# Kernel tuning notes

Hardware: AMD Instinct MI355X
Metric: run time of the kernel (lower is better)

The kernel has to match this reference:

```python
import jax, jax.numpy as jnp
import numpy as np

B, S, DIM, FF = 64, 577, 768, 3072
BLK = 8          # block_shape = (8, 8)
DENSITY = 0.1    # fraction of 8x8 blocks that are nonzero


def _expand_block_mask(m):
    # m: [out//BLK, in//BLK] bool -> [out, in] float mask
    return jnp.repeat(jnp.repeat(m, BLK, axis=0), BLK, axis=1)


def setup_inputs() -> dict:
    key = jax.random.key(0)
    ks = jax.random.split(key, 7)
    x = jax.random.normal(ks[0], (B, S, DIM), dtype=jnp.float32)
    # nn.Linear-style init scale
    W1 = jax.random.normal(ks[1], (FF, DIM), dtype=jnp.float32) / np.sqrt(DIM).astype(np.float32)
    b1 = jax.random.normal(ks[2], (FF,), dtype=jnp.float32) * 0.02
    W2 = jax.random.normal(ks[3], (DIM, FF), dtype=jnp.float32) / np.sqrt(FF).astype(np.float32)
    b2 = jax.random.normal(ks[4], (DIM,), dtype=jnp.float32) * 0.02
    mask1 = jax.random.uniform(ks[5], (FF // BLK, DIM // BLK)) < DENSITY
    mask2 = jax.random.uniform(ks[6], (DIM // BLK, FF // BLK)) < DENSITY
    return {"x": x, "W1": W1, "b1": b1, "W2": W2, "b2": b2,
            "mask1": mask1, "mask2": mask2}


def reference(x, W1, b1, W2, b2, mask1, mask2):
    # fc1: block-sparse linear  y = x @ (W1 * M1)^T + b1
    Wm1 = W1 * _expand_block_mask(mask1).astype(W1.dtype)  # [FF, DIM]
    h = jnp.einsum('bsd,fd->bsf', x, Wm1) + b1             # [B, S, FF]
    h = jax.nn.gelu(h, approximate=False)                  # F.gelu default (exact)
    # fc2: block-sparse linear
    Wm2 = W2 * _expand_block_mask(mask2).astype(W2.dtype)  # [DIM, FF]
    return jnp.einsum('bsf,df->bsd', h, Wm2) + b2          # [B, S, DIM]
```

## Files before the change

### kernel.cpp

```cpp
#include <hip/hip_runtime.h>
#include <hip/hip_bf16.h>


typedef __attribute__((ext_vector_type(8))) short short8;
typedef __attribute__((ext_vector_type(4))) float f32x4;
typedef unsigned long long u64;
typedef unsigned short ushort_t;

#define DIM 768
#define FF 3072
#define NF16 192
#define ND16 48
#define NDB 96
#define NFB 384
#define MR 32
#define NT 1024
#define XP 776
#define HP 1544
#define XSEC (16 * XP)
#define HSEC (16 * HP)

#define S1CAP (NF16 * 96 + 32)
#define S2CAP (ND16 * 2 * 192 + 32)
#define W1S_TOT (S1CAP * 128)
#define W2S_TOT (S2CAP * 128)

#define MFMA __builtin_amdgcn_mfma_f32_16x16x32_bf16

__device__ __forceinline__ float gelu_fast(float v) {
    float t2 = v * fmaf(v * v, -0.10295667f, -2.30235629f);
    return v / (1.0f + exp2f(t2));
}
__device__ __forceinline__ ushort_t f2bs(float f) {
    union { __hip_bfloat16 h; ushort_t u; } cv;
    cv.h = __float2bfloat16(f);
    return cv.u;
}

__global__ __launch_bounds__(64)
void prep_count(const int* __restrict__ mask1, const int* __restrict__ mask2,
                int* __restrict__ off1, int* __restrict__ off2)
{
    const int l = threadIdx.x;
    const int g = blockIdx.x;
    if (g < NF16) {
        const int* r0 = mask1 + (2 * g) * NDB;
        const int* r1 = r0 + NDB;
        bool ua = (r0[l] | r1[l]) != 0;
        u64 ba = __ballot(ua);
        bool ub = (l < 32) && ((r0[64 + l] | r1[64 + l]) != 0);
        u64 bb = __ballot(ub);
        if (l == 0) {
            int cnt = __popcll(ba) + __popcll(bb);
            off1[g + 1] = (cnt + 15) & ~15;
        }
    } else {
        const int G = g - NF16;
        const int* r0 = mask2 + (2 * G) * NFB;
        const int* r1 = r0 + NFB;
        int c0 = 0, c1 = 0;
        #pragma unroll
        for (int p = 0; p < 6; ++p) {
            u64 b = __ballot((r0[p * 64 + l] | r1[p * 64 + l]) != 0);
            if (p < 3) c0 += __popcll(b); else c1 += __popcll(b);
        }
        if (l == 0) {
            off2[0 * ND16 + G + 1] = (c0 + 15) & ~15;
            off2[1 * ND16 + G + 1] = (c1 + 15) & ~15;
        }
    }
}

__global__ __launch_bounds__(64)
void prep_scan(int* __restrict__ off1, int* __restrict__ off2,
               ushort_t* __restrict__ idx1s, ushort_t* __restrict__ idx2s)
{
    if (threadIdx.x == 0) {
        off1[0] = 0;
        for (int i = 0; i < NF16; ++i) off1[i + 1] += off1[i];
        int e = off1[NF16];
        for (int i = 0; i < 32; ++i) idx1s[e + i] = 0;
    } else if (threadIdx.x == 1) {
        off2[0] = 0;
        for (int i = 0; i < 2 * ND16; ++i) off2[i + 1] += off2[i];
        int e = off2[2 * ND16];
        for (int i = 0; i < 32; ++i) idx2s[e + i] = 0;
    }
}

__global__ __launch_bounds__(256)
void prep_gather(const float* __restrict__ W1, const float* __restrict__ W2,
                 const int* __restrict__ mask1, const int* __restrict__ mask2,
                 const int* __restrict__ off1, const int* __restrict__ off2,
                 __hip_bfloat16* __restrict__ w1s, __hip_bfloat16* __restrict__ w2s,
                 ushort_t* __restrict__ idx1s, ushort_t* __restrict__ idx2s)
{
    __shared__ ushort_t sidx[192];
    __shared__ int sc[1];
    const int tid = threadIdx.x;
    const int l = tid & 63;
    const int g = blockIdx.x;

    if (g < NF16) {
        const int F = g;
        const int* r0 = mask1 + (2 * F) * NDB;
        const int* r1 = r0 + NDB;
        if (tid < 64) {
            bool ua = (r0[l] | r1[l]) != 0;
            u64 ba = __ballot(ua);
            bool ub = (l < 32) && ((r0[64 + l] | r1[64 + l]) != 0);
            u64 bb = __ballot(ub);
            int ca = __popcll(ba);
            if (ua) sidx[__popcll(ba & ((1ull << l) - 1ull))] = (ushort_t)l;
            if (ub) sidx[ca + __popcll(bb & ((1ull << l) - 1ull))] = (ushort_t)(64 + l);
            int cnt = ca + __popcll(bb);
            if (l == 0) {
                sc[0] = cnt;
                int cntp = (cnt + 15) & ~15;
                for (int i = cnt; i < cntp && i < 192; ++i) sidx[i] = 0;
            }
        }
        __syncthreads();
        const int cnt = sc[0];
        const int base = off1[F];
        const int cntp = off1[F + 1] - base;
        if (tid < cntp) idx1s[base + tid] = sidx[tid];
        for (int e = tid; e < cntp * 128; e += 256) {
            int slot = e >> 7, r = (e >> 3) & 15, j = e & 7;
            int db = sidx[slot];
            float w = 0.f;
            if (slot < cnt && mask1[(2 * F + (r >> 3)) * NDB + db])
                w = W1[(long)(F * 16 + r) * DIM + db * 8 + j];
            w1s[(long)base * 128 + e] = __float2bfloat16(w);
        }
    } else {
        const int gi = g - NF16;
        const int c = gi / ND16;
        const int G = gi % ND16;
        const int* r0 = mask2 + (2 * G) * NFB;
        const int* r1 = r0 + NFB;
        if (tid < 64) {
            u64 b[3]; int pc[3];
            #pragma unroll
            for (int p = 0; p < 3; ++p) {
                int fb = c * 192 + p * 64 + l;
                b[p] = __ballot((r0[fb] | r1[fb]) != 0);
                pc[p] = __popcll(b[p]);
            }
            int basea = 0;
            #pragma unroll
            for (int p = 0; p < 3; ++p) {
                if ((b[p] >> l) & 1ull)
                    sidx[basea + __popcll(b[p] & ((1ull << l) - 1ull))] = (ushort_t)(p * 64 + l);
                basea += pc[p];
            }
            if (l == 0) {
                int cnt = basea;
                sc[0] = cnt;
                int cntp = (cnt + 15) & ~15;
                for (int i = cnt; i < cntp && i < 192; ++i) sidx[i] = 0;
            }
        }
        __syncthreads();
        const int cnt = sc[0];
        const int base = off2[c * ND16 + G];
        const int cntp = off2[c * ND16 + G + 1] - base;
        if (tid < cntp) idx2s[base + tid] = sidx[tid];
        for (int e = tid; e < cntp * 128; e += 256) {
            int slot = e >> 7, r = (e >> 3) & 15, j = e & 7;
            int lfb = sidx[slot];
            int fb = c * 192 + lfb;
            float w = 0.f;
            if (slot < cnt && mask2[(2 * G + (r >> 3)) * NFB + fb])
                w = W2[(long)(G * 16 + r) * FF + fb * 8 + j];
            w2s[(long)base * 128 + e] = __float2bfloat16(w);
        }
    }
}

#define PREF(BUF, IP, WP, ARR, ROWOFF, SECOFF)                          \
    {                                                                   \
        uint4 q = *(const uint4*)(IP);                                  \
        unsigned dd0 = (lg & 2) ? q.y : q.x;                            \
        unsigned dd1 = (lg & 2) ? q.w : q.z;                            \
        int mo0 = (int)((dd0 >> shsel) & 0xffffu) * 8;                  \
        int mo1 = (int)((dd1 >> shsel) & 0xffffu) * 8;                  \
        BUF##a0 = *(const short8*)&ARR[ROWOFF + mo0];                   \
        BUF##a1 = *(const short8*)&ARR[ROWOFF + SECOFF + mo0];          \
        BUF##a2 = *(const short8*)&ARR[ROWOFF + mo1];                   \
        BUF##a3 = *(const short8*)&ARR[ROWOFF + SECOFF + mo1];          \
        BUF##w0 = *(const short8*)(WP);                                 \
        BUF##w1 = *(const short8*)(WP + 512);                           \
    }

#define PAIRSTEP(IP, WP, ARR, ROWOFF, SECOFF)                           \
    {                                                                   \
        short8 t0 = Aa0, t1 = Aa1, t2 = Aa2, t3 = Aa3, u0 = Aw0, u1 = Aw1; \
        PREF(A, IP, WP, ARR, ROWOFF, SECOFF)                            \
        ca = MFMA(t0, u0, ca, 0, 0, 0); cc = MFMA(t1, u0, cc, 0, 0, 0); \
        cb = MFMA(t2, u1, cb, 0, 0, 0); cd = MFMA(t3, u1, cd, 0, 0, 0); \
    }                                                                   \
    {                                                                   \
        short8 t0 = Ba0, t1 = Ba1, t2 = Ba2, t3 = Ba3, u0 = Bw0, u1 = Bw1; \
        PREF(B, (IP + 8), (WP + 1024), ARR, ROWOFF, SECOFF)             \
        ca = MFMA(t0, u0, ca, 0, 0, 0); cc = MFMA(t1, u0, cc, 0, 0, 0); \
        cb = MFMA(t2, u1, cb, 0, 0, 0); cd = MFMA(t3, u1, cd, 0, 0, 0); \
    }                                                                   \
    IP += 16; WP += 2048; s += 16;

__global__ __launch_bounds__(NT, 4)
void bsffn_main(const float* __restrict__ x,
                const float* __restrict__ pb1, const float* __restrict__ pb2,
                const ushort_t* __restrict__ w1s, const ushort_t* __restrict__ w2s,
                const ushort_t* __restrict__ idx1s, const ushort_t* __restrict__ idx2s,
                const int* __restrict__ off1, const int* __restrict__ off2,
                float* __restrict__ out)
{
    __shared__ __align__(16) ushort_t xs[MR * XP];
    __shared__ __align__(16) ushort_t hs[MR * HP];

    const int tid = threadIdx.x;
    const int wave = tid >> 6;
    const int l = tid & 63;
    const int l15 = l & 15;
    const int lg = l >> 4;
    const int xrow = l15 * XP;
    const int hrow = l15 * HP;
    const int lofs = lg * 128 + l15 * 8;
    const unsigned shsel = (unsigned)((lg & 1) << 4);
    const long rowBase = (long)blockIdx.x * MR;

    {
        const float* xr = x + rowBase * DIM;
        #pragma unroll
        for (int i = 0; i < 3; ++i) {
            int e = tid + i * NT;
            int row = e / 96, c8 = e % 96;
            const float4 v0 = *(const float4*)(xr + row * DIM + c8 * 8);
            const float4 v1 = *(const float4*)(xr + row * DIM + c8 * 8 + 4);
            uint4 wv;
            wv.x = (unsigned)f2bs(v0.x) | ((unsigned)f2bs(v0.y) << 16);
            wv.y = (unsigned)f2bs(v0.z) | ((unsigned)f2bs(v0.w) << 16);
            wv.z = (unsigned)f2bs(v1.x) | ((unsigned)f2bs(v1.y) << 16);
            wv.w = (unsigned)f2bs(v1.z) | ((unsigned)f2bs(v1.w) << 16);
            *(uint4*)&xs[row * XP + c8 * 8] = wv;
        }
    }

    f32x4 acc0[3], acc1[3];
    #pragma unroll
    for (int t = 0; t < 3; ++t) {
        acc0[t] = (f32x4){0.f, 0.f, 0.f, 0.f};
        acc1[t] = (f32x4){0.f, 0.f, 0.f, 0.f};
    }

    __syncthreads();

    for (int chunk = 0; chunk < 2; ++chunk) {
        {
            const int Fbeg = chunk * 96 + wave * 6;
            int s = off1[Fbeg];
            const ushort_t* ip = idx1s + s;
            const ushort_t* wp = w1s + (long)s * 128 + lofs;
            short8 Aa0, Aa1, Aa2, Aa3, Aw0, Aw1, Ba0, Ba1, Ba2, Ba3, Bw0, Bw1;
            PREF(A, ip, wp, xs, xrow, XSEC)
            PREF(B, (ip + 8), (wp + 1024), xs, xrow, XSEC)
            ip += 16; wp += 2048;
            #pragma unroll 1
            for (int j = 0; j < 6; ++j) {
                const int F = Fbeg + j;
                const int gend = off1[F + 1];
                f32x4 ca = {0.f,0.f,0.f,0.f}, cb = ca, cc = ca, cd = ca;
                while (s < gend) { PAIRSTEP(ip, wp, xs, xrow, XSEC) }
                const float bias = pb1[F * 16 + l15];
                const int hcol = (F - chunk * 96) * 16 + l15;
                #pragma unroll
                for (int r = 0; r < 4; ++r) {
                    hs[(lg * 4 + r) * HP + hcol] = f2bs(gelu_fast(ca[r] + cb[r] + bias));
                    hs[HSEC + (lg * 4 + r) * HP + hcol] = f2bs(gelu_fast(cc[r] + cd[r] + bias));
                }
            }
        }
        __syncthreads();

        {
            const int Pbeg = chunk * ND16 + wave * 3;
            int s = off2[Pbeg];
            const ushort_t* ip = idx2s + s;
            const ushort_t* wp = w2s + (long)s * 128 + lofs;
            short8 Aa0, Aa1, Aa2, Aa3, Aw0, Aw1, Ba0, Ba1, Ba2, Ba3, Bw0, Bw1;
            PREF(A, ip, wp, hs, hrow, HSEC)
            PREF(B, (ip + 8), (wp + 1024), hs, hrow, HSEC)
            ip += 16; wp += 2048;
#define FC2G(J)                                                          \
            {                                                            \
                const int gend = off2[Pbeg + (J) + 1];                   \
                f32x4 ca = acc0[J], cc = acc1[J];                        \
                f32x4 cb = {0.f,0.f,0.f,0.f}, cd = cb;                   \
                while (s < gend) { PAIRSTEP(ip, wp, hs, hrow, HSEC) }    \
                acc0[J] = ca + cb; acc1[J] = cc + cd;                    \
            }
            FC2G(0) FC2G(1) FC2G(2)
#undef FC2G
        }
        __syncthreads();
    }

    float* sacc = (float*)hs;
    #pragma unroll
    for (int j = 0; j < 3; ++j) {
        const int d = (wave * 3 + j) * 16 + l15;
        #pragma unroll
        for (int r = 0; r < 4; ++r) {
            sacc[(lg * 4 + r) * 772 + d] = acc0[j][r];
            sacc[(16 + lg * 4 + r) * 772 + d] = acc1[j][r];
        }
    }
    __syncthreads();
    {
        const float4* pb24 = (const float4*)pb2;
        #pragma unroll
        for (int i = 0; i < 6; ++i) {
            int e = tid + i * NT;
            int row = e / 192, c4 = e % 192;
            float4 v = *(const float4*)&sacc[row * 772 + c4 * 4];
            float4 b = pb24[c4];
            v.x += b.x; v.y += b.y; v.z += b.z; v.w += b.w;
            *(float4*)&out[(rowBase + row) * DIM + c4 * 4] = v;
        }
    }
}

extern "C" void kernel_launch(void* const* d_in, const int* in_sizes, int n_in,
                              void* d_out, int out_size, void* d_ws, size_t ws_size,
                              hipStream_t stream) {
    const float* x = (const float*)d_in[0];
    const float* W1 = (const float*)d_in[1];
    const float* b1 = (const float*)d_in[2];
    const float* W2 = (const float*)d_in[3];
    const float* b2 = (const float*)d_in[4];
    const int* mask1 = (const int*)d_in[5];
    const int* mask2 = (const int*)d_in[6];
    float* out = (float*)d_out;

    ushort_t* w1s = (ushort_t*)d_ws;
    ushort_t* w2s = w1s + W1S_TOT;
    ushort_t* idx1s = w2s + W2S_TOT;
    ushort_t* idx2s = idx1s + S1CAP;
    int* off1 = (int*)(idx2s + S2CAP);
    int* off2 = off1 + (NF16 + 1);

    prep_count<<<NF16 + ND16, 64, 0, stream>>>(mask1, mask2, off1, off2);
    prep_scan<<<1, 64, 0, stream>>>(off1, off2, idx1s, idx2s);
    prep_gather<<<NF16 + 2 * ND16, 256, 0, stream>>>(
        W1, W2, mask1, mask2, off1, off2,
        (__hip_bfloat16*)w1s, (__hip_bfloat16*)w2s, idx1s, idx2s);

    const int rows = in_sizes[0] / DIM;
    const int nblk = rows / MR;
    bsffn_main<<<nblk, NT, 0, stream>>>(
        x, b1, b2, w1s, w2s, idx1s, idx2s, off1, off2, out);
}
```

Measured before the change: 347.7 us.

## Switch block-sparse FFN to 32x32x16 MFMA tiles with swizzled LDS

Regroups the packed sparse weights into 32-row feature groups so the main kernel can use 32x32x16 bf16 MFMA instead of 16x16x32. The block drops to 12 waves, each owning 32-wide output tiles. The x and h tiles in LDS get an XOR swizzle to cut bank conflicts. The goal is better operand reuse per instruction and fewer LDS conflicts. The cost is that a 32-row group packs the union of four mask rows instead of two, so more zero blocks get multiplied, and fewer waves per CU are resident.

```diff
diff --git a/kernel.cpp b/kernel.cpp
--- a/kernel.cpp
+++ b/kernel.cpp
@@ -3,29 +3,27 @@
 
 
 typedef __attribute__((ext_vector_type(8))) short short8;
-typedef __attribute__((ext_vector_type(4))) float f32x4;
+typedef __attribute__((ext_vector_type(16))) float f32x16;
 typedef unsigned long long u64;
 typedef unsigned short ushort_t;
 
 #define DIM 768
 #define FF 3072
-#define NF16 192
-#define ND16 48
+#define NF32 96
+#define NG32 24
 #define NDB 96
 #define NFB 384
 #define MR 32
-#define NT 1024
+#define NT 768
 #define XP 776
 #define HP 1544
-#define XSEC (16 * XP)
-#define HSEC (16 * HP)
-
-#define S1CAP (NF16 * 96 + 32)
-#define S2CAP (ND16 * 2 * 192 + 32)
-#define W1S_TOT (S1CAP * 128)
-#define W2S_TOT (S2CAP * 128)
-
-#define MFMA __builtin_amdgcn_mfma_f32_16x16x32_bf16
+
+#define S1CAP (NF32 * 96 + 32)
+#define S2CAP (48 * 192 + 32)
+#define W1S_TOT (S1CAP * 256)
+#define W2S_TOT (S2CAP * 256)
+
+#define MFMA32 __builtin_amdgcn_mfma_f32_32x32x16_bf16
 
 __device__ __forceinline__ float gelu_fast(float v) {
     float t2 = v * fmaf(v * v, -0.10295667f, -2.30235629f);
@@ -43,30 +41,30 @@
 {
     const int l = threadIdx.x;
     const int g = blockIdx.x;
-    if (g < NF16) {
-        const int* r0 = mask1 + (2 * g) * NDB;
-        const int* r1 = r0 + NDB;
-        bool ua = (r0[l] | r1[l]) != 0;
+    if (g < NF32) {
+        const int* r0 = mask1 + (4 * g) * NDB;
+        bool ua = (r0[l] | r0[NDB + l] | r0[2 * NDB + l] | r0[3 * NDB + l]) != 0;
         u64 ba = __ballot(ua);
-        bool ub = (l < 32) && ((r0[64 + l] | r1[64 + l]) != 0);
+        bool ub = (l < 32) &&
+            ((r0[64 + l] | r0[NDB + 64 + l] | r0[2 * NDB + 64 + l] | r0[3 * NDB + 64 + l]) != 0);
         u64 bb = __ballot(ub);
         if (l == 0) {
             int cnt = __popcll(ba) + __popcll(bb);
             off1[g + 1] = (cnt + 15) & ~15;
         }
     } else {
-        const int G = g - NF16;
-        const int* r0 = mask2 + (2 * G) * NFB;
-        const int* r1 = r0 + NFB;
+        const int G = g - NF32;
+        const int* r0 = mask2 + (4 * G) * NFB;
         int c0 = 0, c1 = 0;
         #pragma unroll
         for (int p = 0; p < 6; ++p) {
-            u64 b = __ballot((r0[p * 64 + l] | r1[p * 64 + l]) != 0);
+            int fb = p * 64 + l;
+            u64 b = __ballot((r0[fb] | r0[NFB + fb] | r0[2 * NFB + fb] | r0[3 * NFB + fb]) != 0);
             if (p < 3) c0 += __popcll(b); else c1 += __popcll(b);
         }
         if (l == 0) {
-            off2[0 * ND16 + G + 1] = (c0 + 15) & ~15;
-            off2[1 * ND16 + G + 1] = (c1 + 15) & ~15;
+            off2[0 * NG32 + G + 1] = (c0 + 15) & ~15;
+            off2[1 * NG32 + G + 1] = (c1 + 15) & ~15;
         }
     }
 }
@@ -77,13 +75,13 @@
 {
     if (threadIdx.x == 0) {
         off1[0] = 0;
-        for (int i = 0; i < NF16; ++i) off1[i + 1] += off1[i];
-        int e = off1[NF16];
+        for (int i = 0; i < NF32; ++i) off1[i + 1] += off1[i];
+        int e = off1[NF32];
         for (int i = 0; i < 32; ++i) idx1s[e + i] = 0;
     } else if (threadIdx.x == 1) {
         off2[0] = 0;
-        for (int i = 0; i < 2 * ND16; ++i) off2[i + 1] += off2[i];
-        int e = off2[2 * ND16];
+        for (int i = 0; i < 2 * NG32; ++i) off2[i + 1] += off2[i];
+        int e = off2[2 * NG32];
         for (int i = 0; i < 32; ++i) idx2s[e + i] = 0;
     }
 }
@@ -101,14 +99,14 @@
     const int l = tid & 63;
     const int g = blockIdx.x;
 
-    if (g < NF16) {
+    if (g < NF32) {
         const int F = g;
-        const int* r0 = mask1 + (2 * F) * NDB;
-        const int* r1 = r0 + NDB;
+        const int* r0 = mask1 + (4 * F) * NDB;
         if (tid < 64) {
-            bool ua = (r0[l] | r1[l]) != 0;
+            bool ua = (r0[l] | r0[NDB + l] | r0[2 * NDB + l] | r0[3 * NDB + l]) != 0;
             u64 ba = __ballot(ua);
-            bool ub = (l < 32) && ((r0[64 + l] | r1[64 + l]) != 0);
+            bool ub = (l < 32) &&
+                ((r0[64 + l] | r0[NDB + 64 + l] | r0[2 * NDB + 64 + l] | r0[3 * NDB + 64 + l]) != 0);
             u64 bb = __ballot(ub);
             int ca = __popcll(ba);
             if (ua) sidx[__popcll(ba & ((1ull << l) - 1ull))] = (ushort_t)l;
@@ -125,26 +123,25 @@
         const int base = off1[F];
         const int cntp = off1[F + 1] - base;
         if (tid < cntp) idx1s[base + tid] = sidx[tid];
-        for (int e = tid; e < cntp * 128; e += 256) {
-            int slot = e >> 7, r = (e >> 3) & 15, j = e & 7;
+        for (int e = tid; e < cntp * 256; e += 256) {
+            int slot = e >> 8, c = (e >> 3) & 31, j = e & 7;
             int db = sidx[slot];
             float w = 0.f;
-            if (slot < cnt && mask1[(2 * F + (r >> 3)) * NDB + db])
-                w = W1[(long)(F * 16 + r) * DIM + db * 8 + j];
-            w1s[(long)base * 128 + e] = __float2bfloat16(w);
+            if (slot < cnt && mask1[(4 * F + (c >> 3)) * NDB + db])
+                w = W1[(long)(F * 32 + c) * DIM + db * 8 + j];
+            w1s[(long)(base + slot) * 256 + c * 8 + j] = __float2bfloat16(w);
         }
     } else {
-        const int gi = g - NF16;
-        const int c = gi / ND16;
-        const int G = gi % ND16;
-        const int* r0 = mask2 + (2 * G) * NFB;
-        const int* r1 = r0 + NFB;
+        const int gi = g - NF32;
+        const int c = gi / NG32;
+        const int G = gi % NG32;
+        const int* r0 = mask2 + (4 * G) * NFB;
         if (tid < 64) {
             u64 b[3]; int pc[3];
             #pragma unroll
             for (int p = 0; p < 3; ++p) {
                 int fb = c * 192 + p * 64 + l;
-                b[p] = __ballot((r0[fb] | r1[fb]) != 0);
+                b[p] = __ballot((r0[fb] | r0[NFB + fb] | r0[2 * NFB + fb] | r0[3 * NFB + fb]) != 0);
                 pc[p] = __popcll(b[p]);
             }
             int basea = 0;
@@ -163,52 +160,60 @@
         }
         __syncthreads();
         const int cnt = sc[0];
-        const int base = off2[c * ND16 + G];
-        const int cntp = off2[c * ND16 + G + 1] - base;
+        const int base = off2[c * NG32 + G];
+        const int cntp = off2[c * NG32 + G + 1] - base;
         if (tid < cntp) idx2s[base + tid] = sidx[tid];
-        for (int e = tid; e < cntp * 128; e += 256) {
-            int slot = e >> 7, r = (e >> 3) & 15, j = e & 7;
+        for (int e = tid; e < cntp * 256; e += 256) {
+            int slot = e >> 8, cc = (e >> 3) & 31, j = e & 7;
             int lfb = sidx[slot];
             int fb = c * 192 + lfb;
             float w = 0.f;
-            if (slot < cnt && mask2[(2 * G + (r >> 3)) * NFB + fb])
-                w = W2[(long)(G * 16 + r) * FF + fb * 8 + j];
-            w2s[(long)base * 128 + e] = __float2bfloat16(w);
-        }
-    }
-}
-
-#define PREF(BUF, IP, WP, ARR, ROWOFF, SECOFF)                          \
+            if (slot < cnt && mask2[(4 * G + (cc >> 3)) * NFB + fb])
+                w = W2[(long)(G * 32 + cc) * FF + fb * 8 + j];
+            w2s[(long)(base + slot) * 256 + cc * 8 + j] = __float2bfloat16(w);
+        }
+    }
+}
+
+#define PREF(BUF, IP, WP, ARR, ROWOFF)                                  \
     {                                                                   \
         uint4 q = *(const uint4*)(IP);                                  \
-        unsigned dd0 = (lg & 2) ? q.y : q.x;                            \
-        unsigned dd1 = (lg & 2) ? q.w : q.z;                            \
-        int mo0 = (int)((dd0 >> shsel) & 0xffffu) * 8;                  \
-        int mo1 = (int)((dd1 >> shsel) & 0xffffu) * 8;                  \
-        BUF##a0 = *(const short8*)&ARR[ROWOFF + mo0];                   \
-        BUF##a1 = *(const short8*)&ARR[ROWOFF + SECOFF + mo0];          \
-        BUF##a2 = *(const short8*)&ARR[ROWOFF + mo1];                   \
-        BUF##a3 = *(const short8*)&ARR[ROWOFF + SECOFF + mo1];          \
+        int m0 = (int)((q.x >> hsh) & 0xffffu) ^ rx;                    \
+        int m1 = (int)((q.y >> hsh) & 0xffffu) ^ rx;                    \
+        int m2 = (int)((q.z >> hsh) & 0xffffu) ^ rx;                    \
+        int m3 = (int)((q.w >> hsh) & 0xffffu) ^ rx;                    \
+        BUF##a0 = *(const short8*)&ARR[ROWOFF + m0 * 8];                \
+        BUF##a1 = *(const short8*)&ARR[ROWOFF + m1 * 8];                \
+        BUF##a2 = *(const short8*)&ARR[ROWOFF + m2 * 8];                \
+        BUF##a3 = *(const short8*)&ARR[ROWOFF + m3 * 8];                \
         BUF##w0 = *(const short8*)(WP);                                 \
         BUF##w1 = *(const short8*)(WP + 512);                           \
-    }
-
-#define PAIRSTEP(IP, WP, ARR, ROWOFF, SECOFF)                           \
+        BUF##w2 = *(const short8*)(WP + 1024);                          \
+        BUF##w3 = *(const short8*)(WP + 1536);                          \
+    }
+
+#define PAIRSTEP(IP, WP, ARR, ROWOFF)                                   \
     {                                                                   \
-        short8 t0 = Aa0, t1 = Aa1, t2 = Aa2, t3 = Aa3, u0 = Aw0, u1 = Aw1; \
-        PREF(A, IP, WP, ARR, ROWOFF, SECOFF)                            \
-        ca = MFMA(t0, u0, ca, 0, 0, 0); cc = MFMA(t1, u0, cc, 0, 0, 0); \
-        cb = MFMA(t2, u1, cb, 0, 0, 0); cd = MFMA(t3, u1, cd, 0, 0, 0); \
+        short8 a0 = Aa0, a1 = Aa1, a2 = Aa2, a3 = Aa3;                  \
+        short8 w0 = Aw0, w1 = Aw1, w2 = Aw2, w3 = Aw3;                  \
+        PREF(A, IP, WP, ARR, ROWOFF)                                    \
+        ca = MFMA32(a0, w0, ca, 0, 0, 0);                               \
+        ca = MFMA32(a1, w1, ca, 0, 0, 0);                               \
+        ca = MFMA32(a2, w2, ca, 0, 0, 0);                               \
+        ca = MFMA32(a3, w3, ca, 0, 0, 0);                               \
     }                                                                   \
     {                                                                   \
-        short8 t0 = Ba0, t1 = Ba1, t2 = Ba2, t3 = Ba3, u0 = Bw0, u1 = Bw1; \
-        PREF(B, (IP + 8), (WP + 1024), ARR, ROWOFF, SECOFF)             \
-        ca = MFMA(t0, u0, ca, 0, 0, 0); cc = MFMA(t1, u0, cc, 0, 0, 0); \
-        cb = MFMA(t2, u1, cb, 0, 0, 0); cd = MFMA(t3, u1, cd, 0, 0, 0); \
+        short8 a0 = Ba0, a1 = Ba1, a2 = Ba2, a3 = Ba3;                  \
+        short8 w0 = Bw0, w1 = Bw1, w2 = Bw2, w3 = Bw3;                  \
+        PREF(B, (IP + 8), (WP + 2048), ARR, ROWOFF)                     \
+        cb = MFMA32(a0, w0, cb, 0, 0, 0);                               \
+        cb = MFMA32(a1, w1, cb, 0, 0, 0);                               \
+        cb = MFMA32(a2, w2, cb, 0, 0, 0);                               \
+        cb = MFMA32(a3, w3, cb, 0, 0, 0);                               \
     }                                                                   \
-    IP += 16; WP += 2048; s += 16;
-
-__global__ __launch_bounds__(NT, 4)
+    IP += 16; WP += 4096; s += 16;
+
+__global__ __launch_bounds__(NT)
 void bsffn_main(const float* __restrict__ x,
                 const float* __restrict__ pb1, const float* __restrict__ pb2,
                 const ushort_t* __restrict__ w1s, const ushort_t* __restrict__ w2s,
@@ -222,18 +227,19 @@
     const int tid = threadIdx.x;
     const int wave = tid >> 6;
     const int l = tid & 63;
-    const int l15 = l & 15;
-    const int lg = l >> 4;
-    const int xrow = l15 * XP;
-    const int hrow = l15 * HP;
-    const int lofs = lg * 128 + l15 * 8;
-    const unsigned shsel = (unsigned)((lg & 1) << 4);
+    const int l31 = l & 31;
+    const int lh = l >> 5;
+    const int rx = l31 >> 3;
+    const unsigned hsh = (unsigned)(lh << 4);
+    const int xrow = l31 * XP;
+    const int hrow = l31 * HP;
+    const int wlofs = lh * 256 + l31 * 8;
     const long rowBase = (long)blockIdx.x * MR;
 
     {
         const float* xr = x + rowBase * DIM;
         #pragma unroll
-        for (int i = 0; i < 3; ++i) {
+        for (int i = 0; i < 4; ++i) {
             int e = tid + i * NT;
             int row = e / 96, c8 = e % 96;
             const float4 v0 = *(const float4*)(xr + row * DIM + c8 * 8);
@@ -243,84 +249,96 @@
             wv.y = (unsigned)f2bs(v0.z) | ((unsigned)f2bs(v0.w) << 16);
             wv.z = (unsigned)f2bs(v1.x) | ((unsigned)f2bs(v1.y) << 16);
             wv.w = (unsigned)f2bs(v1.z) | ((unsigned)f2bs(v1.w) << 16);
-            *(uint4*)&xs[row * XP + c8 * 8] = wv;
-        }
-    }
-
-    f32x4 acc0[3], acc1[3];
+            *(uint4*)&xs[row * XP + ((c8 ^ (row >> 3)) * 8)] = wv;
+        }
+    }
+
+    f32x16 accA, accB;
     #pragma unroll
-    for (int t = 0; t < 3; ++t) {
-        acc0[t] = (f32x4){0.f, 0.f, 0.f, 0.f};
-        acc1[t] = (f32x4){0.f, 0.f, 0.f, 0.f};
-    }
+    for (int r = 0; r < 16; ++r) { accA[r] = 0.f; accB[r] = 0.f; }
 
     __syncthreads();
 
     for (int chunk = 0; chunk < 2; ++chunk) {
         {
-            const int Fbeg = chunk * 96 + wave * 6;
+            const int Fbeg = chunk * 48 + wave * 4;
             int s = off1[Fbeg];
             const ushort_t* ip = idx1s + s;
-            const ushort_t* wp = w1s + (long)s * 128 + lofs;
-            short8 Aa0, Aa1, Aa2, Aa3, Aw0, Aw1, Ba0, Ba1, Ba2, Ba3, Bw0, Bw1;
-            PREF(A, ip, wp, xs, xrow, XSEC)
-            PREF(B, (ip + 8), (wp + 1024), xs, xrow, XSEC)
-            ip += 16; wp += 2048;
+            const ushort_t* wp = w1s + (long)s * 256 + wlofs;
+            short8 Aa0, Aa1, Aa2, Aa3, Aw0, Aw1, Aw2, Aw3;
+            short8 Ba0, Ba1, Ba2, Ba3, Bw0, Bw1, Bw2, Bw3;
+            PREF(A, ip, wp, xs, xrow)
+            PREF(B, (ip + 8), (wp + 2048), xs, xrow)
+            ip += 16; wp += 4096;
             #pragma unroll 1
-            for (int j = 0; j < 6; ++j) {
+            for (int j = 0; j < 4; ++j) {
                 const int F = Fbeg + j;
                 const int gend = off1[F + 1];
-                f32x4 ca = {0.f,0.f,0.f,0.f}, cb = ca, cc = ca, cd = ca;
-                while (s < gend) { PAIRSTEP(ip, wp, xs, xrow, XSEC) }
-                const float bias = pb1[F * 16 + l15];
-                const int hcol = (F - chunk * 96) * 16 + l15;
-                #pragma unroll
-                for (int r = 0; r < 4; ++r) {
-                    hs[(lg * 4 + r) * HP + hcol] = f2bs(gelu_fast(ca[r] + cb[r] + bias));
-                    hs[HSEC + (lg * 4 + r) * HP + hcol] = f2bs(gelu_fast(cc[r] + cd[r] + bias));
+                f32x16 ca, cb;
+                #pragma unroll
+                for (int r = 0; r < 16; ++r) { ca[r] = 0.f; cb[r] = 0.f; }
+                while (s < gend) { PAIRSTEP(ip, wp, xs, xrow) }
+                const float bias = pb1[F * 32 + l31];
+                const int hc3 = (F - chunk * 48) * 4 + (l31 >> 3);
+                const int he7 = l31 & 7;
+                #pragma unroll
+                for (int r = 0; r < 16; ++r) {
+                    int rs = (r & 3) + 8 * (r >> 2) + 4 * lh;
+                    float v = gelu_fast(ca[r] + cb[r] + bias);
+                    hs[rs * HP + ((hc3 ^ (r >> 2)) << 3) + he7] = f2bs(v);
                 }
             }
         }
         __syncthreads();
 
         {
-            const int Pbeg = chunk * ND16 + wave * 3;
+            const int Pbeg = chunk * NG32 + wave * 2;
             int s = off2[Pbeg];
             const ushort_t* ip = idx2s + s;
-            const ushort_t* wp = w2s + (long)s * 128 + lofs;
-            short8 Aa0, Aa1, Aa2, Aa3, Aw0, Aw1, Ba0, Ba1, Ba2, Ba3, Bw0, Bw1;
-            PREF(A, ip, wp, hs, hrow, HSEC)
-            PREF(B, (ip + 8), (wp + 1024), hs, hrow, HSEC)
-            ip += 16; wp += 2048;
-#define FC2G(J)                                                          \
-            {                                                            \
-                const int gend = off2[Pbeg + (J) + 1];                   \
-                f32x4 ca = acc0[J], cc = acc1[J];                        \
-                f32x4 cb = {0.f,0.f,0.f,0.f}, cd = cb;                   \
-                while (s < gend) { PAIRSTEP(ip, wp, hs, hrow, HSEC) }    \
-                acc0[J] = ca + cb; acc1[J] = cc + cd;                    \
-            }
-            FC2G(0) FC2G(1) FC2G(2)
-#undef FC2G
+            const ushort_t* wp = w2s + (long)s * 256 + wlofs;
+            short8 Aa0, Aa1, Aa2, Aa3, Aw0, Aw1, Aw2, Aw3;
+            short8 Ba0, Ba1, Ba2, Ba3, Bw0, Bw1, Bw2, Bw3;
+            PREF(A, ip, wp, hs, hrow)
+            PREF(B, (ip + 8), (wp + 2048), hs, hrow)
+            ip += 16; wp += 4096;
+            {
+                const int gend = off2[Pbeg + 1];
+                f32x16 ca = accA, cb;
+                #pragma unroll
+                for (int r = 0; r < 16; ++r) cb[r] = 0.f;
+                while (s < gend) { PAIRSTEP(ip, wp, hs, hrow) }
+                #pragma unroll
+                for (int r = 0; r < 16; ++r) accA[r] = ca[r] + cb[r];
+            }
+            {
+                const int gend = off2[Pbeg + 2];
+                f32x16 ca = accB, cb;
+                #pragma unroll
+                for (int r = 0; r < 16; ++r) cb[r] = 0.f;
+                while (s < gend) { PAIRSTEP(ip, wp, hs, hrow) }
+                #pragma unroll
+                for (int r = 0; r < 16; ++r) accB[r] = ca[r] + cb[r];
+            }
         }
         __syncthreads();
     }
 
     float* sacc = (float*)hs;
-    #pragma unroll
-    for (int j = 0; j < 3; ++j) {
-        const int d = (wave * 3 + j) * 16 + l15;
+    {
+        const int d0 = (wave * 2) * 32 + l31;
+        const int d1 = (wave * 2 + 1) * 32 + l31;
         #pragma unroll
-        for (int r = 0; r < 4; ++r) {
-            sacc[(lg * 4 + r) * 772 + d] = acc0[j][r];
-            sacc[(16 + lg * 4 + r) * 772 + d] = acc1[j][r];
+        for (int r = 0; r < 16; ++r) {
+            int rs = (r & 3) + 8 * (r >> 2) + 4 * lh;
+            sacc[rs * 772 + d0] = accA[r];
+            sacc[rs * 772 + d1] = accB[r];
         }
     }
     __syncthreads();
     {
         const float4* pb24 = (const float4*)pb2;
         #pragma unroll
-        for (int i = 0; i < 6; ++i) {
+        for (int i = 0; i < 8; ++i) {
             int e = tid + i * NT;
             int row = e / 192, c4 = e % 192;
             float4 v = *(const float4*)&sacc[row * 772 + c4 * 4];
@@ -348,11 +366,11 @@
     ushort_t* idx1s = w2s + W2S_TOT;
     ushort_t* idx2s = idx1s + S1CAP;
     int* off1 = (int*)(idx2s + S2CAP);
-    int* off2 = off1 + (NF16 + 1);
-
-    prep_count<<<NF16 + ND16, 64, 0, stream>>>(mask1, mask2, off1, off2);
+    int* off2 = off1 + (NF32 + 1);
+
+    prep_count<<<NF32 + NG32, 64, 0, stream>>>(mask1, mask2, off1, off2);
     prep_scan<<<1, 64, 0, stream>>>(off1, off2, idx1s, idx2s);
-    prep_gather<<<NF16 + 2 * ND16, 256, 0, stream>>>(
+    prep_gather<<<NF32 + 2 * NG32, 256, 0, stream>>>(
         W1, W2, mask1, mask2, off1, off2,
         (__hip_bfloat16*)w1s, (__hip_bfloat16*)w2s, idx1s, idx2s);
 
```

New measurement: 349.4 us. No clear change (+0.5%).
